# Kernel optimization log

Hardware: AMD Instinct MI355X
Metric: run time of the kernel (lower is better)

## Reference

```python
import jax, jax.numpy as jnp
import numpy as np

NUM_EMBEDDINGS = 1024
EMBEDDING_DIM = 256
COMMITMENT_COST = 0.25


def setup_inputs() -> dict:
    key = jax.random.key(0)
    k1, k2 = jax.random.split(key)
    inputs = jax.random.normal(k1, (32, EMBEDDING_DIM, 32, 32), dtype=jnp.float32)
    # nn.Embedding weight init: uniform(-1/K, 1/K)
    embeddings = (jax.random.uniform(k2, (NUM_EMBEDDINGS, EMBEDDING_DIM), dtype=jnp.float32) * 2.0 - 1.0) / NUM_EMBEDDINGS
    return {"inputs": inputs, "embeddings": embeddings}


def reference(inputs, embeddings):
    B, D, H, W = inputs.shape
    K = embeddings.shape[0]
    # [B,D,H,W] -> [N,D] with N = B*H*W
    flat = jnp.transpose(inputs, (0, 2, 3, 1)).reshape(-1, D)
    distances = (jnp.sum(flat * flat, axis=1, keepdims=True)
                 + jnp.sum(embeddings * embeddings, axis=1)
                 - 2.0 * jnp.matmul(flat, embeddings.T))
    encoding_indices = jnp.argmin(distances, axis=1)  # [N]
    # gather codebook vectors (same math as one-hot @ embeddings)
    quantized = embeddings[encoding_indices]  # [N,D]
    quantized = quantized.reshape(B, H, W, D).transpose(0, 3, 1, 2)  # [B,D,H,W]
    e_latent_loss = jnp.mean((jax.lax.stop_gradient(quantized) - inputs) ** 2)
    q_latent_loss = jnp.mean((quantized - jax.lax.stop_gradient(inputs)) ** 2)
    loss = q_latent_loss + COMMITMENT_COST * e_latent_loss
    # straight-through estimator
    quantized_st = inputs + jax.lax.stop_gradient(quantized - inputs)
    # perplexity from one-hot average (counts / N)
    counts = jnp.zeros((K,), dtype=flat.dtype).at[encoding_indices].add(1.0)
    avg_probs = counts / flat.shape[0]
    perplexity = jnp.exp(-jnp.sum(avg_probs * jnp.log(avg_probs + 1e-10)))
    return quantized_st, loss, perplexity, encoding_indices.reshape(B, H, W)
```

## Files before the change

kernel.cpp:

```cpp
#include <hip/hip_runtime.h>


#define NROWS 32768
#define CAPA 16384
#define CAPB 8192
#define GAP_TAU 1e-4f

typedef __attribute__((ext_vector_type(8))) short short8;
typedef __attribute__((ext_vector_type(8))) unsigned short ushort8;
typedef __attribute__((ext_vector_type(4))) float f32x4;

struct Top4 { float v0, v1, v2, v3; int i0, i1, i2; };

__device__ __forceinline__ void top4_init(Top4& t) {
    t.v0 = t.v1 = t.v2 = t.v3 = 3.4e38f;
    t.i0 = t.i1 = t.i2 = 0x7fffffff;
}
__device__ __forceinline__ void top4_insert(Top4& t, float cv, int ci) {
    if (cv < t.v3) {
        if (cv < t.v2) {
            t.v3 = t.v2;
            if (cv < t.v1) {
                t.v2 = t.v1; t.i2 = t.i1;
                if (cv < t.v0) { t.v1 = t.v0; t.i1 = t.i0; t.v0 = cv; t.i0 = ci; }
                else           { t.v1 = cv; t.i1 = ci; }
            } else { t.v2 = cv; t.i2 = ci; }
        } else { t.v3 = cv; }
    }
}
__device__ __forceinline__ void top4_merge(Top4& t, const Top4& o) {
    top4_insert(t, o.v0, o.i0);
    top4_insert(t, o.v1, o.i1);
    top4_insert(t, o.v2, o.i2);
    t.v3 = fminf(t.v3, o.v3);
}

__device__ __forceinline__ unsigned short bf16_rne(float v) {
    unsigned int u = __float_as_uint(v);
    return (unsigned short)((u + 0x7fffu + ((u >> 16) & 1u)) >> 16);
}
__device__ __forceinline__ float bf16_to_f(unsigned short h) {
    return __uint_as_float(((unsigned int)h) << 16);
}

__device__ __forceinline__ void gl16(const void* g, void* l) {
    __builtin_amdgcn_global_load_lds(
        (const __attribute__((address_space(1))) unsigned int*)g,
        (__attribute__((address_space(3))) unsigned int*)l, 16, 0, 0);
}

template <int STRIDE>
__device__ __forceinline__ float np_sumsq256(const float* __restrict__ p) {
    float half[2];
#pragma unroll
    for (int h = 0; h < 2; ++h) {
        float r[8];
#pragma unroll
        for (int j = 0; j < 8; ++j) {
            const float v = p[(size_t)(h * 128 + j) * STRIDE];
            r[j] = __fmul_rn(v, v);
        }
        for (int i = 8; i < 128; i += 8) {
#pragma unroll
            for (int j = 0; j < 8; ++j) {
                const float v = p[(size_t)(h * 128 + i + j) * STRIDE];
                r[j] = __fadd_rn(r[j], __fmul_rn(v, v));
            }
        }
        half[h] = __fadd_rn(__fadd_rn(__fadd_rn(r[0], r[1]), __fadd_rn(r[2], r[3])),
                            __fadd_rn(__fadd_rn(r[4], r[5]), __fadd_rn(r[6], r[7])));
    }
    return __fadd_rn(half[0], half[1]);
}

__global__ void prep_kernel(const float* __restrict__ emb, const float* __restrict__ x,
                            float* __restrict__ ee, float* __restrict__ xx,
                            unsigned short* __restrict__ EhT, unsigned short* __restrict__ ElT,
                            unsigned short* __restrict__ XhT, unsigned short* __restrict__ XlT,
                            float* __restrict__ wzero) {
    if (blockIdx.x >= 388) {
        for (int i = threadIdx.x; i < 1088; i += 256) wzero[i] = 0.f;
        return;
    }
    if (blockIdx.x < 4) {
        const int k = blockIdx.x * 256 + threadIdx.x;
        ee[k] = np_sumsq256<1>(emb + (size_t)k * 256);
        return;
    }
    if (blockIdx.x >= 260) {
        const int n = (blockIdx.x - 260) * 256 + threadIdx.x;
        const int b = n >> 10, p = n & 1023;
        const float* xb = x + (size_t)b * 262144 + p;
        const int kk = (n >> 1) & 3;
        float r[8];
        float half0 = 0.f, half1 = 0.f;
        for (int dc = 0; dc < 8; ++dc) {
            float v[32];
#pragma unroll
            for (int j = 0; j < 32; ++j)
                v[j] = xb[(size_t)(dc * 32 + j) * 1024];
            if ((dc & 3) == 0) {
#pragma unroll
                for (int j = 0; j < 8; ++j) r[j] = __fmul_rn(v[j], v[j]);
#pragma unroll
                for (int g = 1; g < 4; ++g)
#pragma unroll
                    for (int j = 0; j < 8; ++j)
                        r[j] = __fadd_rn(r[j], __fmul_rn(v[g * 8 + j], v[g * 8 + j]));
            } else {
#pragma unroll
                for (int g = 0; g < 4; ++g)
#pragma unroll
                    for (int j = 0; j < 8; ++j)
                        r[j] = __fadd_rn(r[j], __fmul_rn(v[g * 8 + j], v[g * 8 + j]));
            }
            if ((dc & 3) == 3) {
                const float s = __fadd_rn(
                    __fadd_rn(__fadd_rn(r[0], r[1]), __fadd_rn(r[2], r[3])),
                    __fadd_rn(__fadd_rn(r[4], r[5]), __fadd_rn(r[6], r[7])));
                if (dc == 3) half0 = s; else half1 = s;
            }
            const size_t xrow = ((size_t)dc * NROWS + n) * 32;
#pragma unroll
            for (int g = 0; g < 4; ++g) {
                ushort8 H, L;
#pragma unroll
                for (int j = 0; j < 8; ++j) {
                    const float vv = v[g * 8 + j];
                    const unsigned int u = __float_as_uint(vv);
                    H[j] = (unsigned short)(u >> 16);
                    const float rr = vv - __uint_as_float(u & 0xFFFF0000u);
                    L[j] = (unsigned short)(__float_as_uint(rr) >> 16);
                }
                *(ushort8*)(XhT + xrow + (g ^ kk) * 8) = H;
                *(ushort8*)(XlT + xrow + (g ^ kk) * 8) = L;
            }
        }
        xx[n] = __fadd_rn(half0, half1);
        return;
    }
    const int eid = (blockIdx.x - 4) * 256 + threadIdx.x;
    const int code = eid >> 6;
    const int d0 = (eid & 63) * 4;
    float4 v = *(const float4*)(emb + (size_t)code * 256 + d0);
    const float vv[4] = {v.x, v.y, v.z, v.w};
    unsigned short h[4], l[4];
#pragma unroll
    for (int i = 0; i < 4; ++i) {
        h[i] = bf16_rne(vv[i]);
        l[i] = bf16_rne(vv[i] - bf16_to_f(h[i]));
    }
    const int kk = (code >> 1) & 3;
    const int slot = (d0 & 31) >> 3;
    const int within = (d0 & 31) & 7;
    const size_t o = ((size_t)(d0 >> 5) * 1024 + code) * 32
                   + (size_t)((slot ^ kk) * 8 + within);
    *(ushort4*)(EhT + o) = make_ushort4(h[0], h[1], h[2], h[3]);
    *(ushort4*)(ElT + o) = make_ushort4(l[0], l[1], l[2], l[3]);
}

__global__ __launch_bounds__(256, 4)
void mfma_argmin_kernel(const unsigned short* __restrict__ XhT, const unsigned short* __restrict__ XlT,
                        const unsigned short* __restrict__ EhT, const unsigned short* __restrict__ ElT,
                        const float* __restrict__ ee, const float* __restrict__ xx,
                        float* __restrict__ pv0, float* __restrict__ pv1,
                        float* __restrict__ pv2, float* __restrict__ pv3,
                        int* __restrict__ pi0, int* __restrict__ pi1, int* __restrict__ pi2) {
    __shared__ __attribute__((aligned(16))) unsigned short Eh_s[4096];
    __shared__ __attribute__((aligned(16))) unsigned short El_s[4096];
    __shared__ __attribute__((aligned(16))) unsigned short Xh_s[4096];
    __shared__ __attribute__((aligned(16))) unsigned short Xl_s[4096];
    __shared__ float eeLds[128];
    __shared__ float mV0[128], mV1[128], mV2[128], mV3[128];
    __shared__ int   mI0[128], mI1[128], mI2[128];

    const int t = threadIdx.x;
    const int w = t >> 6, lane = t & 63;
    const int lane15 = lane & 15, quad = lane >> 4;
    const int nblk = blockIdx.x & 255, cblk = blockIdx.x >> 8;
    const int n0 = nblk * 128, c0 = cblk * 128;

    if (t < 128) eeLds[t] = ee[c0 + t];

    const int fslot = (quad ^ ((lane15 >> 1) & 3)) * 8;
    int eoffs[4], xoffs[4];
#pragma unroll
    for (int i = 0; i < 4; ++i)
        eoffs[i] = ((w >> 1) * 64 + i * 16 + lane15) * 32 + fslot;
#pragma unroll
    for (int j = 0; j < 4; ++j)
        xoffs[j] = ((w & 1) * 64 + j * 16 + lane15) * 32 + fslot;

    f32x4 acc[4][4];
#pragma unroll
    for (int i = 0; i < 4; ++i)
#pragma unroll
        for (int j = 0; j < 4; ++j) acc[i][j] = (f32x4){0.f, 0.f, 0.f, 0.f};

    for (int dc = 0; dc < 8; ++dc) {
        if (dc) __syncthreads();
        const size_t xoff = ((size_t)dc * NROWS + n0) * 32;
        const size_t eoff = ((size_t)dc * 1024 + c0) * 32;
#pragma unroll
        for (int k = 0; k < 2; ++k) {
            const int id = k * 256 + t;
            const int ldso = (k * 256 + w * 64) * 8;
            gl16(XhT + xoff + (size_t)id * 8, &Xh_s[ldso]);
            gl16(XlT + xoff + (size_t)id * 8, &Xl_s[ldso]);
            gl16(EhT + eoff + (size_t)id * 8, &Eh_s[ldso]);
            gl16(ElT + eoff + (size_t)id * 8, &El_s[ldso]);
        }
        __syncthreads();
        short8 ah[4], al[4], bh[4], bl[4];
#pragma unroll
        for (int i = 0; i < 4; ++i) {
            ah[i] = *(const short8*)&Eh_s[eoffs[i]];
            al[i] = *(const short8*)&El_s[eoffs[i]];
        }
#pragma unroll
        for (int j = 0; j < 4; ++j) {
            bh[j] = *(const short8*)&Xh_s[xoffs[j]];
            bl[j] = *(const short8*)&Xl_s[xoffs[j]];
        }
#pragma unroll
        for (int i = 0; i < 4; ++i)
#pragma unroll
            for (int j = 0; j < 4; ++j) {
                acc[i][j] = __builtin_amdgcn_mfma_f32_16x16x32_bf16(al[i], bh[j], acc[i][j], 0, 0, 0);
                acc[i][j] = __builtin_amdgcn_mfma_f32_16x16x32_bf16(ah[i], bl[j], acc[i][j], 0, 0, 0);
                acc[i][j] = __builtin_amdgcn_mfma_f32_16x16x32_bf16(ah[i], bh[j], acc[i][j], 0, 0, 0);
            }
    }

    Top4 tj[4];
#pragma unroll
    for (int j = 0; j < 4; ++j) {
        const float xxv = xx[n0 + (w & 1) * 64 + j * 16 + lane15];
        Top4 tt; top4_init(tt);
#pragma unroll
        for (int i = 0; i < 4; ++i)
#pragma unroll
            for (int r = 0; r < 4; ++r) {
                const int cl = (w >> 1) * 64 + i * 16 + quad * 4 + r;
                const float t1 = __fadd_rn(xxv, eeLds[cl]);
                const float s = __fmaf_rn(-2.0f, acc[i][j][r], t1);
                top4_insert(tt, s, c0 + cl);
            }
#pragma unroll
        for (int off = 16; off <= 32; off <<= 1) {
            Top4 o;
            o.v0 = __shfl_xor(tt.v0, off, 64); o.i0 = __shfl_xor(tt.i0, off, 64);
            o.v1 = __shfl_xor(tt.v1, off, 64); o.i1 = __shfl_xor(tt.i1, off, 64);
            o.v2 = __shfl_xor(tt.v2, off, 64); o.i2 = __shfl_xor(tt.i2, off, 64);
            o.v3 = __shfl_xor(tt.v3, off, 64);
            top4_merge(tt, o);
        }
        tj[j] = tt;
    }
    __syncthreads();
    if (w >= 2 && quad == 0) {
#pragma unroll
        for (int j = 0; j < 4; ++j) {
            const int idx = (w & 1) * 64 + j * 16 + lane15;
            mV0[idx] = tj[j].v0; mV1[idx] = tj[j].v1; mV2[idx] = tj[j].v2; mV3[idx] = tj[j].v3;
            mI0[idx] = tj[j].i0; mI1[idx] = tj[j].i1; mI2[idx] = tj[j].i2;
        }
    }
    __syncthreads();
    if (w < 2 && quad == 0) {
#pragma unroll
        for (int j = 0; j < 4; ++j) {
            const int idx = w * 64 + j * 16 + lane15;
            Top4 tt = tj[j];
            Top4 o;
            o.v0 = mV0[idx]; o.v1 = mV1[idx]; o.v2 = mV2[idx]; o.v3 = mV3[idx];
            o.i0 = mI0[idx]; o.i1 = mI1[idx]; o.i2 = mI2[idx];
            top4_merge(tt, o);
            mV0[idx] = tt.v0; mV1[idx] = tt.v1; mV2[idx] = tt.v2; mV3[idx] = tt.v3;
            mI0[idx] = tt.i0; mI1[idx] = tt.i1; mI2[idx] = tt.i2;
        }
    }
    __syncthreads();
    if (t < 128) {
        const size_t g = (size_t)cblk * NROWS + n0 + t;
        pv0[g] = mV0[t]; pv1[g] = mV1[t]; pv2[g] = mV2[t]; pv3[g] = mV3[t];
        pi0[g] = mI0[t]; pi1[g] = mI1[t]; pi2[g] = mI2[t];
    }
}

__global__ void combine_kernel(const float* __restrict__ pv0, const float* __restrict__ pv1,
                               const float* __restrict__ pv2, const float* __restrict__ pv3,
                               const int* __restrict__ pi0, const int* __restrict__ pi1,
                               const int* __restrict__ pi2,
                               int* __restrict__ fidx, float* __restrict__ outIdx,
                               int* __restrict__ counts,
                               int* __restrict__ listA, int* __restrict__ nA,
                               int* __restrict__ listB, int* __restrict__ nB) {
    const int n = blockIdx.x * blockDim.x + threadIdx.x;
    if (n >= NROWS) return;
    float v0[8], v1[8], v2[8]; int i0[8], i1[8], i2[8];
    float b1 = 3.4e38f, v4m = 3.4e38f;
#pragma unroll
    for (int s = 0; s < 8; ++s) {
        const size_t g = (size_t)s * NROWS + n;
        v0[s] = pv0[g]; v1[s] = pv1[g]; v2[s] = pv2[g];
        i0[s] = pi0[g]; i1[s] = pi1[g]; i2[s] = pi2[g];
        b1 = fminf(b1, v0[s]);
        v4m = fminf(v4m, pv3[g]);
    }
    if (v4m - b1 < GAP_TAU) {
        const int s = atomicAdd(nB, 1);
        if (s < CAPB) { listB[s] = n; return; }
    } else {
        int ks[24]; int cnt = 0;
#pragma unroll
        for (int s = 0; s < 8; ++s) {
            if (v0[s] - b1 < GAP_TAU) ks[cnt++] = i0[s];
            if (v1[s] - b1 < GAP_TAU) ks[cnt++] = i1[s];
            if (v2[s] - b1 < GAP_TAU) ks[cnt++] = i2[s];
        }
        if (cnt > 1) {
            const int slot = atomicAdd(nA, 1);
            if (slot < CAPA) {
                int* e = listA + (size_t)slot * 32;
                e[0] = n; e[1] = cnt;
                for (int c = 0; c < cnt; ++c) e[2 + c] = ks[c];
                return;
            }
            const int s2 = atomicAdd(nB, 1);
            if (s2 < CAPB) { listB[s2] = n; return; }
        }
        const int bi = ks[0];
        fidx[n] = bi;
        outIdx[n] = (float)bi;
        atomicAdd(&counts[bi], 1);
        return;
    }
    int bi = 0x7fffffff;
#pragma unroll
    for (int s = 0; s < 8; ++s) if (v0[s] == b1 && i0[s] < bi) bi = i0[s];
    fidx[n] = bi; outIdx[n] = (float)bi; atomicAdd(&counts[bi], 1);
}

__global__ __launch_bounds__(256)
void resolve_kernel(const float* __restrict__ x, const float* __restrict__ emb,
                    const float* __restrict__ ee, const float* __restrict__ xx,
                    const int* __restrict__ listA, const int* __restrict__ nA,
                    const int* __restrict__ listB, const int* __restrict__ nB,
                    int* __restrict__ fidx, float* __restrict__ outIdx,
                    int* __restrict__ counts) {
    __shared__ float xrow[256];
    __shared__ float bV[4];
    __shared__ int   bI[4];
    if (blockIdx.x < 512) {
        int total = *nA; if (total > CAPA) total = CAPA;
        const int sub = threadIdx.x >> 5;
        const int li  = threadIdx.x & 31;
        for (int e = blockIdx.x * 8 + sub; e < total; e += 512 * 8) {
            const int* ent = listA + (size_t)e * 32;
            const int n = ent[0], cnt = ent[1];
            float s = 3.4e38f; int k = 0x7fffffff;
            if (li < cnt) {
                k = ent[2 + li];
                const int b = n >> 10, p = n & 1023;
                const float* xr = x + (size_t)b * 262144 + p;
                const float* er = emb + (size_t)k * 256;
                float dot = 0.f;
#pragma unroll 8
                for (int d = 0; d < 256; ++d)
                    dot = __fmaf_rn(er[d], xr[(size_t)d * 1024], dot);
                s = __fmaf_rn(-2.0f, dot, __fadd_rn(xx[n], ee[k]));
            }
#pragma unroll
            for (int off = 1; off < 32; off <<= 1) {
                const float ov = __shfl_xor(s, off, 32);
                const int   ok = __shfl_xor(k, off, 32);
                if (ov < s || (ov == s && ok < k)) { s = ov; k = ok; }
            }
            if (li == 0) { fidx[n] = k; outIdx[n] = (float)k; atomicAdd(&counts[k], 1); }
        }
        return;
    }
    int total = *nB; if (total > CAPB) total = CAPB;
    for (int wq = (int)blockIdx.x - 512; wq < total; wq += 64) {
        const int n = listB[wq];
        const int b = n >> 10, p = n & 1023;
        const float* xb = x + (size_t)b * 262144 + p;
        xrow[threadIdx.x] = xb[(size_t)threadIdx.x * 1024];
        __syncthreads();
        const float xxn = xx[n];
        float best = 3.4e38f; int bi = 0x7fffffff;
        for (int k = threadIdx.x; k < 1024; k += 256) {
            const float* e = emb + (size_t)k * 256;
            float dot = 0.f;
            for (int d = 0; d < 256; ++d) dot = __fmaf_rn(e[d], xrow[d], dot);
            const float t1 = __fadd_rn(xxn, ee[k]);
            const float s = __fmaf_rn(-2.0f, dot, t1);
            if (s < best) { best = s; bi = k; }
        }
        for (int off = 32; off > 0; off >>= 1) {
            const float ov = __shfl_down(best, off, 64);
            const int   oi = __shfl_down(bi,   off, 64);
            if (ov < best || (ov == best && oi < bi)) { best = ov; bi = oi; }
        }
        const int lane = threadIdx.x & 63, wv = threadIdx.x >> 6;
        if (lane == 0) { bV[wv] = best; bI[wv] = bi; }
        __syncthreads();
        if (threadIdx.x == 0) {
            float bb = bV[0]; int ii = bI[0];
            for (int i = 1; i < 4; ++i)
                if (bV[i] < bb || (bV[i] == bb && bI[i] < ii)) { bb = bV[i]; ii = bI[i]; }
            fidx[n] = ii;
            outIdx[n] = (float)ii;
            atomicAdd(&counts[ii], 1);
        }
        __syncthreads();
    }
}

__global__ __launch_bounds__(256)
void quantize_kernel(const float* __restrict__ x, const float* __restrict__ emb,
                     const int* __restrict__ fidx, float* __restrict__ out,
                     float* __restrict__ sumsq) {
    const int tid = blockIdx.x * 256 + threadIdx.x;
    const int dchunk = tid >> 15;
    const int n = tid & 32767;
    const int b = n >> 10, p = n & 1023;
    const int d0 = dchunk * 64;
    const int k = fidx[n];
    const float4* er = (const float4*)(emb + (size_t)k * 256 + d0);
    const float* xr = x + (size_t)b * 262144 + (size_t)d0 * 1024 + p;
    float* orow = out + (size_t)b * 262144 + (size_t)d0 * 1024 + p;
    float loc = 0.f;
#pragma unroll
    for (int j = 0; j < 16; ++j) {
        const float4 qv = er[j];
        const float q[4] = {qv.x, qv.y, qv.z, qv.w};
#pragma unroll
        for (int i = 0; i < 4; ++i) {
            const size_t off = (size_t)(j * 4 + i) * 1024;
            const float xv = xr[off];
            const float e = q[i] - xv;
            orow[off] = xv + e;
            loc = fmaf(e, e, loc);
        }
    }
    for (int off = 32; off > 0; off >>= 1) loc += __shfl_down(loc, off, 64);
    __shared__ float red[4];
    const int lane = threadIdx.x & 63, wv = threadIdx.x >> 6;
    if (lane == 0) red[wv] = loc;
    __syncthreads();
    if (threadIdx.x == 0) atomicAdd(sumsq, red[0] + red[1] + red[2] + red[3]);
}

__global__ void finalize_kernel(const int* __restrict__ counts, const float* __restrict__ sumsq,
                                float* __restrict__ outScalars) {
    const int k = threadIdx.x;
    const float p = (float)counts[k] * (1.0f / 32768.0f);
    float term = p * logf(p + 1e-10f);
    for (int off = 32; off > 0; off >>= 1) term += __shfl_down(term, off, 64);
    __shared__ float red[16];
    const int lane = k & 63, wv = k >> 6;
    if (lane == 0) red[wv] = term;
    __syncthreads();
    if (k == 0) {
        float s = 0.f;
        for (int i = 0; i < 16; ++i) s += red[i];
        const float m = sumsq[0] * (1.0f / 8388608.0f);
        outScalars[0] = 1.25f * m;
        outScalars[1] = expf(-s);
    }
}

extern "C" void kernel_launch(void* const* d_in, const int* in_sizes, int n_in,
                              void* d_out, int out_size, void* d_ws, size_t ws_size,
                              hipStream_t stream) {
    const float* x   = (const float*)d_in[0];
    const float* emb = (const float*)d_in[1];
    float* out = (float*)d_out;
    float* W   = (float*)d_ws;
    float* sumsq = W;
    int*   nA    = (int*)(W + 1);
    int*   nB    = (int*)(W + 2);
    int*   counts = (int*)(W + 64);
    float* ee    = W + 1088;
    float* xx    = W + 2112;
    float* pv0   = W + 34880;
    float* pv1   = W + 297024;
    float* pv2   = W + 559168;
    float* pv3   = W + 821312;
    int*   pi0   = (int*)(W + 1083456);
    int*   pi1   = (int*)(W + 1345600);
    int*   pi2   = (int*)(W + 1607744);
    int*   listA = (int*)(W + 1869888);
    int*   listB = (int*)(W + 2394176);
    unsigned short* EhT = (unsigned short*)(W + 2402368);
    unsigned short* ElT = (unsigned short*)(W + 2533440);
    int*   fidx  = (int*)(W + 2664512);
    unsigned short* XhT = (unsigned short*)(W + 2697280);
    unsigned short* XlT = (unsigned short*)(W + 6891584);

    prep_kernel<<<389, 256, 0, stream>>>(emb, x, ee, xx, EhT, ElT, XhT, XlT, W);
    mfma_argmin_kernel<<<2048, 256, 0, stream>>>(XhT, XlT, EhT, ElT, ee, xx,
                                                 pv0, pv1, pv2, pv3, pi0, pi1, pi2);
    combine_kernel<<<128, 256, 0, stream>>>(pv0, pv1, pv2, pv3, pi0, pi1, pi2,
                                            fidx, out + 8388610, counts, listA, nA, listB, nB);
    resolve_kernel<<<576, 256, 0, stream>>>(x, emb, ee, xx, listA, nA, listB, nB,
                                            fidx, out + 8388610, counts);
    quantize_kernel<<<512, 256, 0, stream>>>(x, emb, fidx, out, sumsq);
    finalize_kernel<<<1, 1024, 0, stream>>>(counts, sumsq, out + 8388608);
}
```

Baseline: 214.5 us.

## Load MFMA operands directly from global memory instead of staging through LDS

The argmin GEMM kernel stops staging the bf16 hi/lo tiles of X and E through shared memory with global_load_lds and per-chunk barriers. Each lane now loads its short8 fragments straight from global memory, relying on L1/L2 to serve the data shared between waves. The loop over D-chunks is unrolled by two so loads from the next chunk can overlap the MFMAs of the current one, and launch bounds are relaxed from 4 to 3 blocks per SIMD to allow more registers. In exchange, each wave re-fetches operands that other waves in the block also read, which raises cache traffic, and occupancy may drop.

```diff
diff --git a/kernel.cpp b/kernel.cpp
--- a/kernel.cpp
+++ b/kernel.cpp
@@ -43,12 +43,6 @@
     return __uint_as_float(((unsigned int)h) << 16);
 }
 
-__device__ __forceinline__ void gl16(const void* g, void* l) {
-    __builtin_amdgcn_global_load_lds(
-        (const __attribute__((address_space(1))) unsigned int*)g,
-        (__attribute__((address_space(3))) unsigned int*)l, 16, 0, 0);
-}
-
 template <int STRIDE>
 __device__ __forceinline__ float np_sumsq256(const float* __restrict__ p) {
     float half[2];
@@ -159,17 +153,13 @@
     *(ushort4*)(ElT + o) = make_ushort4(l[0], l[1], l[2], l[3]);
 }
 
-__global__ __launch_bounds__(256, 4)
+__global__ __launch_bounds__(256, 3)
 void mfma_argmin_kernel(const unsigned short* __restrict__ XhT, const unsigned short* __restrict__ XlT,
                         const unsigned short* __restrict__ EhT, const unsigned short* __restrict__ ElT,
                         const float* __restrict__ ee, const float* __restrict__ xx,
                         float* __restrict__ pv0, float* __restrict__ pv1,
                         float* __restrict__ pv2, float* __restrict__ pv3,
                         int* __restrict__ pi0, int* __restrict__ pi1, int* __restrict__ pi2) {
-    __shared__ __attribute__((aligned(16))) unsigned short Eh_s[4096];
-    __shared__ __attribute__((aligned(16))) unsigned short El_s[4096];
-    __shared__ __attribute__((aligned(16))) unsigned short Xh_s[4096];
-    __shared__ __attribute__((aligned(16))) unsigned short Xl_s[4096];
     __shared__ float eeLds[128];
     __shared__ float mV0[128], mV1[128], mV2[128], mV3[128];
     __shared__ int   mI0[128], mI1[128], mI2[128];
@@ -183,44 +173,31 @@
     if (t < 128) eeLds[t] = ee[c0 + t];
 
     const int fslot = (quad ^ ((lane15 >> 1) & 3)) * 8;
-    int eoffs[4], xoffs[4];
+    const size_t ebase = (size_t)(c0 + (w >> 1) * 64 + lane15) * 32 + fslot;
+    const size_t xbase = (size_t)(n0 + (w & 1) * 64 + lane15) * 32 + fslot;
+
+    f32x4 acc[4][4];
 #pragma unroll
     for (int i = 0; i < 4; ++i)
-        eoffs[i] = ((w >> 1) * 64 + i * 16 + lane15) * 32 + fslot;
-#pragma unroll
-    for (int j = 0; j < 4; ++j)
-        xoffs[j] = ((w & 1) * 64 + j * 16 + lane15) * 32 + fslot;
-
-    f32x4 acc[4][4];
-#pragma unroll
-    for (int i = 0; i < 4; ++i)
 #pragma unroll
         for (int j = 0; j < 4; ++j) acc[i][j] = (f32x4){0.f, 0.f, 0.f, 0.f};
 
+#pragma unroll 2
     for (int dc = 0; dc < 8; ++dc) {
-        if (dc) __syncthreads();
-        const size_t xoff = ((size_t)dc * NROWS + n0) * 32;
-        const size_t eoff = ((size_t)dc * 1024 + c0) * 32;
-#pragma unroll
-        for (int k = 0; k < 2; ++k) {
-            const int id = k * 256 + t;
-            const int ldso = (k * 256 + w * 64) * 8;
-            gl16(XhT + xoff + (size_t)id * 8, &Xh_s[ldso]);
-            gl16(XlT + xoff + (size_t)id * 8, &Xl_s[ldso]);
-            gl16(EhT + eoff + (size_t)id * 8, &Eh_s[ldso]);
-            gl16(ElT + eoff + (size_t)id * 8, &El_s[ldso]);
-        }
-        __syncthreads();
+        const unsigned short* Eh = EhT + (size_t)dc * (1024 * 32) + ebase;
+        const unsigned short* El = ElT + (size_t)dc * (1024 * 32) + ebase;
+        const unsigned short* Xh = XhT + (size_t)dc * ((size_t)NROWS * 32) + xbase;
+        const unsigned short* Xl = XlT + (size_t)dc * ((size_t)NROWS * 32) + xbase;
         short8 ah[4], al[4], bh[4], bl[4];
 #pragma unroll
         for (int i = 0; i < 4; ++i) {
-            ah[i] = *(const short8*)&Eh_s[eoffs[i]];
-            al[i] = *(const short8*)&El_s[eoffs[i]];
+            ah[i] = *(const short8*)(Eh + (size_t)i * 512);
+            al[i] = *(const short8*)(El + (size_t)i * 512);
         }
 #pragma unroll
         for (int j = 0; j < 4; ++j) {
-            bh[j] = *(const short8*)&Xh_s[xoffs[j]];
-            bl[j] = *(const short8*)&Xl_s[xoffs[j]];
+            bh[j] = *(const short8*)(Xh + (size_t)j * 512);
+            bl[j] = *(const short8*)(Xl + (size_t)j * 512);
         }
 #pragma unroll
         for (int i = 0; i < 4; ++i)
@@ -231,6 +208,8 @@
                 acc[i][j] = __builtin_amdgcn_mfma_f32_16x16x32_bf16(ah[i], bh[j], acc[i][j], 0, 0, 0);
             }
     }
+
+    __syncthreads();
 
     Top4 tj[4];
 #pragma unroll
```

Measured after the change: 223.1 us. 4.0% more time.

## Split K-chunk loads into two stages to overlap global loads with MFMA

Applied to the files above, without the earlier changes.

The loop now splits each d-chunk's four LDS tile loads into two halves. Stage A loads El and Xh, stage B loads Eh and Xl. The El*Xh MFMAs run while the Eh/Xl loads are in flight, and the next chunk's El/Xh loads are issued while the Eh*Xl and Eh*Xh MFMAs run. This hides global-to-LDS latency behind tensor math. The cost is a second __syncthreads per iteration and MFMA ordering that depends on which data has arrived. The accumulation order changes slightly, which could perturb near-tie argmin results.

```diff
diff --git a/kernel.cpp b/kernel.cpp
--- a/kernel.cpp
+++ b/kernel.cpp
@@ -197,39 +197,62 @@
 #pragma unroll
         for (int j = 0; j < 4; ++j) acc[i][j] = (f32x4){0.f, 0.f, 0.f, 0.f};
 
-    for (int dc = 0; dc < 8; ++dc) {
-        if (dc) __syncthreads();
+    auto STAGE_A = [&](int dc) {
         const size_t xoff = ((size_t)dc * NROWS + n0) * 32;
         const size_t eoff = ((size_t)dc * 1024 + c0) * 32;
 #pragma unroll
         for (int k = 0; k < 2; ++k) {
             const int id = k * 256 + t;
             const int ldso = (k * 256 + w * 64) * 8;
+            gl16(ElT + eoff + (size_t)id * 8, &El_s[ldso]);
             gl16(XhT + xoff + (size_t)id * 8, &Xh_s[ldso]);
+        }
+    };
+    auto STAGE_B = [&](int dc) {
+        const size_t xoff = ((size_t)dc * NROWS + n0) * 32;
+        const size_t eoff = ((size_t)dc * 1024 + c0) * 32;
+#pragma unroll
+        for (int k = 0; k < 2; ++k) {
+            const int id = k * 256 + t;
+            const int ldso = (k * 256 + w * 64) * 8;
+            gl16(EhT + eoff + (size_t)id * 8, &Eh_s[ldso]);
             gl16(XlT + xoff + (size_t)id * 8, &Xl_s[ldso]);
-            gl16(EhT + eoff + (size_t)id * 8, &Eh_s[ldso]);
-            gl16(ElT + eoff + (size_t)id * 8, &El_s[ldso]);
-        }
+        }
+    };
+
+    STAGE_A(0);
+    __syncthreads();
+
+    for (int dc = 0; dc < 8; ++dc) {
+        STAGE_B(dc);
+        short8 al[4], bh[4];
+#pragma unroll
+        for (int i = 0; i < 4; ++i) al[i] = *(const short8*)&El_s[eoffs[i]];
+#pragma unroll
+        for (int j = 0; j < 4; ++j) bh[j] = *(const short8*)&Xh_s[xoffs[j]];
+#pragma unroll
+        for (int i = 0; i < 4; ++i)
+#pragma unroll
+            for (int j = 0; j < 4; ++j)
+                acc[i][j] = __builtin_amdgcn_mfma_f32_16x16x32_bf16(al[i], bh[j], acc[i][j], 0, 0, 0);
         __syncthreads();
-        short8 ah[4], al[4], bh[4], bl[4];
-#pragma unroll
-        for (int i = 0; i < 4; ++i) {
-            ah[i] = *(const short8*)&Eh_s[eoffs[i]];
-            al[i] = *(const short8*)&El_s[eoffs[i]];
-        }
-#pragma unroll
-        for (int j = 0; j < 4; ++j) {
-            bh[j] = *(const short8*)&Xh_s[xoffs[j]];
-            bl[j] = *(const short8*)&Xl_s[xoffs[j]];
-        }
+        if (dc < 7) STAGE_A(dc + 1);
+        short8 ah[4], bl[4];
+#pragma unroll
+        for (int i = 0; i < 4; ++i) ah[i] = *(const short8*)&Eh_s[eoffs[i]];
+#pragma unroll
+        for (int j = 0; j < 4; ++j) bl[j] = *(const short8*)&Xl_s[xoffs[j]];
 #pragma unroll
         for (int i = 0; i < 4; ++i)
 #pragma unroll
-            for (int j = 0; j < 4; ++j) {
-                acc[i][j] = __builtin_amdgcn_mfma_f32_16x16x32_bf16(al[i], bh[j], acc[i][j], 0, 0, 0);
+            for (int j = 0; j < 4; ++j)
                 acc[i][j] = __builtin_amdgcn_mfma_f32_16x16x32_bf16(ah[i], bl[j], acc[i][j], 0, 0, 0);
+#pragma unroll
+        for (int i = 0; i < 4; ++i)
+#pragma unroll
+            for (int j = 0; j < 4; ++j)
                 acc[i][j] = __builtin_amdgcn_mfma_f32_16x16x32_bf16(ah[i], bh[j], acc[i][j], 0, 0, 0);
-            }
+        __syncthreads();
     }
 
     Top4 tj[4];
```

Result: no change. 210.7 us (-1.8%).
